# Optimization experiments

Hardware: AMD Instinct MI355X
Metric: run time of the kernel (lower is better)

Reference implementation:

```python
import jax, jax.numpy as jnp
import numpy as np

B, S, D = 8, 2048, 1024

def setup_inputs() -> dict:
    key = jax.random.key(0)
    ks = jax.random.split(key, 7)
    x = jax.random.normal(ks[0], (B, S, D), dtype=jnp.float32)
    s = 1.0 / np.sqrt(D)
    Wq = jax.random.normal(ks[1], (D, D), dtype=jnp.float32) * s
    bq = jax.random.normal(ks[2], (D,), dtype=jnp.float32) * 0.01
    Wk = jax.random.normal(ks[3], (D, D), dtype=jnp.float32) * s
    bk = jax.random.normal(ks[4], (D,), dtype=jnp.float32) * 0.01
    Wv = jax.random.normal(ks[5], (D, D), dtype=jnp.float32) * s
    bv = jax.random.normal(ks[6], (D,), dtype=jnp.float32) * 0.01
    return {"x": x, "Wq": Wq, "bq": bq, "Wk": Wk, "bk": bk, "Wv": Wv, "bv": bv}

def reference(x, Wq, bq, Wk, bk, Wv, bv):
    # QKV projections: [B,S,D]
    Q = jnp.einsum('bsd,de->bse', x, Wq) + bq
    K = jnp.einsum('bsd,de->bse', x, Wk) + bk
    V = jnp.einsum('bsd,de->bse', x, Wv) + bv
    scale = 1.0 / jnp.sqrt(jnp.asarray(Q.shape[-1], Q.dtype))
    attn = jnp.einsum('bqd,bkd->bqk', Q, K) * scale  # [B,S,S]
    attn = jax.nn.softmax(attn, axis=-1)
    return jnp.einsum('bqk,bkd->bqd', attn, V)
```

## Files before the change

### kernel.cpp

```cpp
#include <hip/hip_runtime.h>
#include <cstdint>


#define Bb 8
#define Ss 2048
#define Dd 1024

typedef unsigned short ushort_t;
typedef __attribute__((ext_vector_type(8))) short short8;
typedef __attribute__((ext_vector_type(4))) float floatx4;

__device__ inline ushort_t f2bf(float f) {
    unsigned int u = __float_as_uint(f);
    unsigned int r = (u + 0x7fffu + ((u >> 16) & 1u)) >> 16;
    return (ushort_t)r;
}
__device__ inline float bf2f(ushort_t u) {
    return __uint_as_float(((unsigned int)u) << 16);
}

__device__ inline floatx4 mfma16(short8 a, short8 b, floatx4 c) {
    return __builtin_amdgcn_mfma_f32_16x16x32_bf16(a, b, c, 0, 0, 0);
}

__device__ inline void gload16(const void* g, void* l) {
    __builtin_amdgcn_global_load_lds(
        (const __attribute__((address_space(1))) void*)g,
        (__attribute__((address_space(3))) void*)l, 16, 0, 0);
}

__device__ __attribute__((always_inline)) void gemm_core256(
    const ushort_t* __restrict__ A, const ushort_t* __restrict__ B,
    int K, int lda, int ldb, int m0, int n0, int tid,
    ushort_t* lds, floatx4 acc[8][4])
{
    const int lane = tid & 63;
    const int wave = tid >> 6;
    const int l3   = lane >> 3;
    const int kc   = ((lane & 7) ^ l3) * 8;

    const ushort_t* aS[2][2];
    const ushort_t* bS[2][2];
#pragma unroll
    for (int i = 0; i < 2; i++) {
#pragma unroll
        for (int g = 0; g < 2; g++) {
            const int r = i * 128 + g * 64 + wave * 8 + l3;
            aS[g][i] = A + (size_t)(m0 + r) * lda + kc;
        }
#pragma unroll
        for (int nh = 0; nh < 2; nh++) {
            const int c = wave + i * 8;
            const int r = (c >> 2) * 64 + nh * 32 + (c & 3) * 8 + l3;
            bS[nh][i] = B + (size_t)(n0 + r) * ldb + kc;
        }
    }

    const int jA   = (wave >> 2) * 64 + (lane & 15);
    const int jB   = (wave & 3) * 32 + (lane & 15);
    const int swz0 = (((lane >> 4) + 0) ^ (lane & 7)) * 8;
    const int swz1 = (((lane >> 4) + 4) ^ (lane & 7)) * 8;

#define STG(DST, REGI, SRC, KOFS)                                             \
    do {                                                                      \
        gload16(SRC[0] + (KOFS), (DST) + (REGI) * 8192 + wave * 512);         \
        gload16(SRC[1] + (KOFS), (DST) + (REGI) * 8192 + (wave + 8) * 512);   \
    } while (0)

#define PHASE(MH, NH, STGSTMT, VMSTMT)                                        \
    do {                                                                      \
        const ushort_t* ba  = cb + (MH) * 8192;                               \
        const ushort_t* bb2 = cb + (2 + (NH)) * 8192;                         \
        short8 af[4][2], bf[2][2];                                            \
        _Pragma("unroll")                                                     \
        for (int mi = 0; mi < 4; mi++) {                                      \
            af[mi][0] = *(const short8*)&ba[(jA + mi * 16) * 64 + swz0];      \
            af[mi][1] = *(const short8*)&ba[(jA + mi * 16) * 64 + swz1];      \
        }                                                                     \
        _Pragma("unroll")                                                     \
        for (int ni = 0; ni < 2; ni++) {                                      \
            bf[ni][0] = *(const short8*)&bb2[(jB + ni * 16) * 64 + swz0];     \
            bf[ni][1] = *(const short8*)&bb2[(jB + ni * 16) * 64 + swz1];     \
        }                                                                     \
        STGSTMT;                                                              \
        __builtin_amdgcn_sched_barrier(0);                                    \
        __builtin_amdgcn_s_barrier();                                         \
        asm volatile("s_waitcnt lgkmcnt(0)" ::: "memory");                    \
        __builtin_amdgcn_sched_barrier(0);                                    \
        __builtin_amdgcn_s_setprio(1);                                        \
        _Pragma("unroll")                                                     \
        for (int ks = 0; ks < 2; ks++)                                        \
            _Pragma("unroll")                                                 \
            for (int mi = 0; mi < 4; mi++)                                    \
                _Pragma("unroll")                                             \
                for (int ni = 0; ni < 2; ni++)                                \
                    acc[(MH) * 4 + mi][(NH) * 2 + ni] = mfma16(               \
                        af[mi][ks], bf[ni][ks],                               \
                        acc[(MH) * 4 + mi][(NH) * 2 + ni]);                   \
        __builtin_amdgcn_s_setprio(0);                                        \
        __builtin_amdgcn_sched_barrier(0);                                    \
        VMSTMT;                                                               \
        __builtin_amdgcn_s_barrier();                                         \
        __builtin_amdgcn_sched_barrier(0);                                    \
    } while (0)

    STG(lds, 0, aS[0], 0);
    STG(lds, 1, aS[1], 0);
    STG(lds, 2, bS[0], 0);
    STG(lds, 3, bS[1], 0);
    STG(lds + 32768, 2, bS[0], 64);
    STG(lds + 32768, 0, aS[0], 64);
    asm volatile("s_waitcnt vmcnt(4)" ::: "memory");
    __builtin_amdgcn_s_barrier();
    __builtin_amdgcn_sched_barrier(0);

    const int NT = K >> 6;
    for (int t = 0; t < NT; t++) {
        const ushort_t* cb = lds + (t & 1) * 32768;
        ushort_t* nb = lds + ((t + 1) & 1) * 32768;
        ushort_t* sb = lds + (t & 1) * 32768;
        const int k1 = (t + 1 < NT ? t + 1 : 0) << 6;
        const int k2 = (t + 2 < NT ? t + 2 : 0) << 6;
        PHASE(0, 0, STG(nb, 1, aS[1], k1), (void)0);
        PHASE(1, 0, STG(nb, 3, bS[1], k1), (void)0);
        PHASE(0, 1, STG(sb, 2, bS[0], k2), (void)0);
        PHASE(1, 1, STG(sb, 0, aS[0], k2),
              asm volatile("s_waitcnt vmcnt(4)" ::: "memory"));
    }
    asm volatile("s_waitcnt vmcnt(0)" ::: "memory");
#undef PHASE
#undef STG
}

template <int EPI>
__global__ __launch_bounds__(512, 2) void gemm256(
    const ushort_t* __restrict__ A, const ushort_t* __restrict__ B,
    void* __restrict__ Cv, float* __restrict__ aux,
    int K, int lda, int ldb, int ldc,
    size_t strideA, size_t strideB, size_t strideC)
{
    const int z = blockIdx.z;
    A += (size_t)z * strideA;
    B += (size_t)z * strideB;
    const int m0 = blockIdx.y * 256;
    const int n0 = blockIdx.x * 256;

    __shared__ __align__(16) ushort_t lds[2 * 4 * 8192];

    floatx4 acc[8][4] = {};
    gemm_core256(A, B, K, lda, ldb, m0, n0, (int)threadIdx.x, lds, acc);

    const int lane = threadIdx.x & 63;
    const int wave = threadIdx.x >> 6;
    const int row0 = m0 + (wave >> 2) * 128 + (lane >> 4) * 4;
    const int col0 = n0 + (wave & 3) * 64 + (lane & 15);

    if (EPI == 0) {
        ushort_t* Cb = (ushort_t*)Cv;
        float bval[4];
#pragma unroll
        for (int nf = 0; nf < 4; nf++) bval[nf] = aux[col0 + nf * 16];
#pragma unroll
        for (int mf = 0; mf < 8; mf++)
#pragma unroll
            for (int i = 0; i < 4; i++) {
                const size_t ro = (size_t)(row0 + mf * 16 + i) * ldc;
#pragma unroll
                for (int nf = 0; nf < 4; nf++)
                    Cb[ro + col0 + nf * 16] = f2bf(acc[mf][nf][i] + bval[nf]);
            }
    } else if (EPI == 1) {
        ushort_t* Cb = (ushort_t*)Cv + (size_t)z * strideC;
        float* ls = aux + z * Ss;
        float rs[8][4];
#pragma unroll
        for (int mf = 0; mf < 8; mf++)
#pragma unroll
            for (int i = 0; i < 4; i++) rs[mf][i] = 0.f;
#pragma unroll
        for (int mf = 0; mf < 8; mf++)
#pragma unroll
            for (int i = 0; i < 4; i++) {
                const size_t ro = (size_t)(row0 + mf * 16 + i) * ldc;
#pragma unroll
                for (int nf = 0; nf < 4; nf++) {
                    const ushort_t o = f2bf(__expf(acc[mf][nf][i] * 0.03125f));
                    Cb[ro + col0 + nf * 16] = o;
                    rs[mf][i] += bf2f(o);
                }
            }
#pragma unroll
        for (int mf = 0; mf < 8; mf++)
#pragma unroll
            for (int i = 0; i < 4; i++) {
                float s = rs[mf][i];
                s += __shfl_xor(s, 1);
                s += __shfl_xor(s, 2);
                s += __shfl_xor(s, 4);
                s += __shfl_xor(s, 8);
                rs[mf][i] = s;
            }
        if ((lane & 15) == 0) {
#pragma unroll
            for (int mf = 0; mf < 8; mf++)
#pragma unroll
                for (int i = 0; i < 4; i++)
                    atomicAdd(&ls[row0 + mf * 16 + i], rs[mf][i]);
        }
    } else {
        float* Cf = (float*)Cv + (size_t)z * strideC;
#pragma unroll
        for (int mf = 0; mf < 8; mf++)
#pragma unroll
            for (int i = 0; i < 4; i++) {
                const int gr = row0 + mf * 16 + i;
                const float iv = 1.0f / aux[z * Ss + gr];
#pragma unroll
                for (int nf = 0; nf < 4; nf++)
                    Cf[(size_t)gr * ldc + col0 + nf * 16] = acc[mf][nf][i] * iv;
            }
    }
}

__global__ __launch_bounds__(256) void vtrans(
    const ushort_t* __restrict__ QKVb, ushort_t* __restrict__ Vt)
{
    __shared__ __align__(16) ushort_t tile[64][72];
    const int t = blockIdx.x;
    const int z = t >> 9, rem = t & 511;
    const int d0 = (rem & 15) * 64, s0 = (rem >> 4) * 64;
    const int tid = threadIdx.x;
    const int rr = tid >> 3;
    const int c8 = (tid & 7) * 8;
#pragma unroll
    for (int i = 0; i < 2; i++) {
        const int s = s0 + rr + i * 32;
        uint4 v = *(const uint4*)&QKVb[((size_t)(z * Ss + s)) * 3072 + 2048 + d0 + c8];
        *(uint4*)&tile[rr + i * 32][c8] = v;
    }
    __syncthreads();
#pragma unroll
    for (int i = 0; i < 2; i++) {
        const int d = rr + i * 32;
        ushort_t u[8];
#pragma unroll
        for (int j = 0; j < 8; j++) u[j] = tile[c8 + j][d];
        *(uint4*)&Vt[(size_t)z * Dd * Ss + (size_t)(d0 + d) * Ss + s0 + c8] =
            *(const uint4*)u;
    }
}

__global__ __launch_bounds__(256) void prep(
    const float* __restrict__ x,
    const float* __restrict__ W0, const float* __restrict__ W1,
    const float* __restrict__ W2,
    const float* __restrict__ bq, const float* __restrict__ bk,
    const float* __restrict__ bv,
    ushort_t* __restrict__ xb, ushort_t* __restrict__ Wall,
    float* __restrict__ ball)
{
    const int bid = blockIdx.x;
    const int tid = threadIdx.x;

    if (bid < 8192) {
        const size_t i = (size_t)bid * 256 + tid;
        const float4* p = (const float4*)x + i * 2;
        float4 a = p[0], b = p[1];
        ushort_t u[8];
        u[0]=f2bf(a.x); u[1]=f2bf(a.y); u[2]=f2bf(a.z); u[3]=f2bf(a.w);
        u[4]=f2bf(b.x); u[5]=f2bf(b.y); u[6]=f2bf(b.z); u[7]=f2bf(b.w);
        *(uint4*)(xb + i * 8) = *(const uint4*)u;
    } else if (bid < 8960) {
        const int t = bid - 8192;
        const int z = t >> 8;
        const float* W = (z == 0) ? W0 : (z == 1) ? W1 : W2;
        ushort_t* Wt = Wall + (size_t)z * Dd * Dd;
        __shared__ float tt[64][65];
        const int n0 = ((t >> 4) & 15) * 64, k0 = (t & 15) * 64;
        const int r  = tid >> 4;
        const int c4 = (tid & 15) * 4;
#pragma unroll
        for (int i = 0; i < 4; i++) {
            float4 v = *(const float4*)&W[(size_t)(k0 + r + i * 16) * Dd + n0 + c4];
            tt[r + i * 16][c4 + 0] = v.x;
            tt[r + i * 16][c4 + 1] = v.y;
            tt[r + i * 16][c4 + 2] = v.z;
            tt[r + i * 16][c4 + 3] = v.w;
        }
        __syncthreads();
#pragma unroll
        for (int i = 0; i < 4; i++) {
            const int rn = r + i * 16;
            ushort_t u[4];
#pragma unroll
            for (int j = 0; j < 4; j++) u[j] = f2bf(tt[c4 + j][rn]);
            *(uint2*)&Wt[(size_t)(n0 + rn) * Dd + k0 + c4] = *(const uint2*)u;
        }
    } else {
#pragma unroll
        for (int j = 0; j < 12; j++) {
            const int idx = j * 256 + tid;
            float v = (idx < 1024) ? bq[idx]
                    : (idx < 2048) ? bk[idx - 1024] : bv[idx - 2048];
            ball[idx] = v;
        }
    }
}

extern "C" void kernel_launch(void* const* d_in, const int* in_sizes, int n_in,
                              void* d_out, int out_size, void* d_ws, size_t ws_size,
                              hipStream_t stream)
{
    const float* x  = (const float*)d_in[0];
    const float* Wq = (const float*)d_in[1];
    const float* bq = (const float*)d_in[2];
    const float* Wk = (const float*)d_in[3];
    const float* bk = (const float*)d_in[4];
    const float* Wv = (const float*)d_in[5];
    const float* bv = (const float*)d_in[6];
    float* out = (float*)d_out;

    char* ws = (char*)d_ws;
    const size_t MB = 1u << 20;
    ushort_t* xb   = (ushort_t*)(ws);
    ushort_t* Vt   = (ushort_t*)(ws);
    ushort_t* QKVb = (ushort_t*)(ws + 32 * MB);
    ushort_t* Pb   = (ushort_t*)(ws + 128 * MB);
    float*    lsum = (float*)(ws + 192 * MB);
    ushort_t* Wall = (ushort_t*)d_out;
    float*    ball = (float*)((char*)d_out + 6 * MB);

    prep<<<8961, 256, 0, stream>>>(x, Wq, Wk, Wv, bq, bk, bv, xb, Wall, ball);

    dim3 g1(3072 / 256, 16384 / 256, 1);
    gemm256<0><<<g1, 512, 0, stream>>>(xb, Wall, QKVb, ball,
                                       Dd, Dd, Dd, 3072, 0, 0, 0);

    hipMemsetAsync(lsum, 0, (size_t)Bb * Ss * sizeof(float), stream);
    vtrans<<<4096, 256, 0, stream>>>(QKVb, Vt);
    dim3 g2(Ss / 256, Ss / 256, Bb);
    gemm256<1><<<g2, 512, 0, stream>>>(QKVb, QKVb + 1024, Pb, lsum,
                                       Dd, 3072, 3072, Ss,
                                       (size_t)Ss * 3072, (size_t)Ss * 3072,
                                       (size_t)Ss * Ss);

    dim3 g3(Dd / 256, Ss / 256, Bb);
    gemm256<3><<<g3, 512, 0, stream>>>(Pb, Vt, out, lsum,
                                       Ss, Ss, Ss, Dd,
                                       (size_t)Ss * Ss, (size_t)Dd * Ss,
                                       (size_t)Ss * Dd);
}
```

Before: 405.2 us.

## Reuse LDS fragments across GEMM phases via serpentine quadrant order

Hoists the A/B fragment registers out of each phase and reorders the four quadrant phases (00,10,11,01) so each phase reloads only one operand half from LDS instead of both. This cuts LDS read traffic per K-tile. The prefetch schedule is reshuffled so each freed LDS slot is refilled right after its last reader. It risks a race if any slot is overwritten while a later phase still reads it.

```diff
diff --git a/kernel.cpp b/kernel.cpp
--- a/kernel.cpp
+++ b/kernel.cpp
@@ -60,6 +60,8 @@
     const int jB   = (wave & 3) * 32 + (lane & 15);
     const int swz0 = (((lane >> 4) + 0) ^ (lane & 7)) * 8;
     const int swz1 = (((lane >> 4) + 4) ^ (lane & 7)) * 8;
+
+    short8 aF[4][2], bF[2][2];
 
 #define STG(DST, REGI, SRC, KOFS)                                             \
     do {                                                                      \
@@ -67,39 +69,46 @@
         gload16(SRC[1] + (KOFS), (DST) + (REGI) * 8192 + (wave + 8) * 512);   \
     } while (0)
 
-#define PHASE(MH, NH, STGSTMT, VMSTMT)                                        \
+#define RD_A(QM)                                                              \
+    _Pragma("unroll")                                                         \
+    for (int mi = 0; mi < 4; mi++) {                                          \
+        const ushort_t* pA_ = cb + (QM) * 8192 + (jA + mi * 16) * 64;         \
+        aF[mi][0] = *(const short8*)&pA_[swz0];                               \
+        aF[mi][1] = *(const short8*)&pA_[swz1];                               \
+    }
+
+#define RD_B(QN)                                                              \
+    _Pragma("unroll")                                                         \
+    for (int ni = 0; ni < 2; ni++) {                                          \
+        const ushort_t* pB_ = cb + (2 + (QN)) * 8192 + (jB + ni * 16) * 64;   \
+        bF[ni][0] = *(const short8*)&pB_[swz0];                               \
+        bF[ni][1] = *(const short8*)&pB_[swz1];                               \
+    }
+
+#define MM(QM, QN)                                                            \
+    _Pragma("unroll")                                                         \
+    for (int ks = 0; ks < 2; ks++)                                            \
+        _Pragma("unroll")                                                     \
+        for (int mi = 0; mi < 4; mi++)                                        \
+            _Pragma("unroll")                                                 \
+            for (int ni = 0; ni < 2; ni++)                                    \
+                acc[(QM) * 4 + mi][(QN) * 2 + ni] =                           \
+                    mfma16(aF[mi][ks], bF[ni][ks],                            \
+                           acc[(QM) * 4 + mi][(QN) * 2 + ni]);
+
+#define PHASE(RDS, MMS, STGS, VMS)                                            \
     do {                                                                      \
-        const ushort_t* ba  = cb + (MH) * 8192;                               \
-        const ushort_t* bb2 = cb + (2 + (NH)) * 8192;                         \
-        short8 af[4][2], bf[2][2];                                            \
-        _Pragma("unroll")                                                     \
-        for (int mi = 0; mi < 4; mi++) {                                      \
-            af[mi][0] = *(const short8*)&ba[(jA + mi * 16) * 64 + swz0];      \
-            af[mi][1] = *(const short8*)&ba[(jA + mi * 16) * 64 + swz1];      \
-        }                                                                     \
-        _Pragma("unroll")                                                     \
-        for (int ni = 0; ni < 2; ni++) {                                      \
-            bf[ni][0] = *(const short8*)&bb2[(jB + ni * 16) * 64 + swz0];     \
-            bf[ni][1] = *(const short8*)&bb2[(jB + ni * 16) * 64 + swz1];     \
-        }                                                                     \
-        STGSTMT;                                                              \
+        RDS                                                                   \
+        STGS;                                                                 \
         __builtin_amdgcn_sched_barrier(0);                                    \
         __builtin_amdgcn_s_barrier();                                         \
         asm volatile("s_waitcnt lgkmcnt(0)" ::: "memory");                    \
         __builtin_amdgcn_sched_barrier(0);                                    \
         __builtin_amdgcn_s_setprio(1);                                        \
-        _Pragma("unroll")                                                     \
-        for (int ks = 0; ks < 2; ks++)                                        \
-            _Pragma("unroll")                                                 \
-            for (int mi = 0; mi < 4; mi++)                                    \
-                _Pragma("unroll")                                             \
-                for (int ni = 0; ni < 2; ni++)                                \
-                    acc[(MH) * 4 + mi][(NH) * 2 + ni] = mfma16(               \
-                        af[mi][ks], bf[ni][ks],                               \
-                        acc[(MH) * 4 + mi][(NH) * 2 + ni]);                   \
+        MMS                                                                   \
         __builtin_amdgcn_s_setprio(0);                                        \
         __builtin_amdgcn_sched_barrier(0);                                    \
-        VMSTMT;                                                               \
+        VMS;                                                                  \
         __builtin_amdgcn_s_barrier();                                         \
         __builtin_amdgcn_sched_barrier(0);                                    \
     } while (0)
@@ -109,7 +118,7 @@
     STG(lds, 2, bS[0], 0);
     STG(lds, 3, bS[1], 0);
     STG(lds + 32768, 2, bS[0], 64);
-    STG(lds + 32768, 0, aS[0], 64);
+    STG(lds + 32768, 1, aS[1], 64);
     asm volatile("s_waitcnt vmcnt(4)" ::: "memory");
     __builtin_amdgcn_s_barrier();
     __builtin_amdgcn_sched_barrier(0);
@@ -121,14 +130,17 @@
         ushort_t* sb = lds + (t & 1) * 32768;
         const int k1 = (t + 1 < NT ? t + 1 : 0) << 6;
         const int k2 = (t + 2 < NT ? t + 2 : 0) << 6;
-        PHASE(0, 0, STG(nb, 1, aS[1], k1), (void)0);
-        PHASE(1, 0, STG(nb, 3, bS[1], k1), (void)0);
-        PHASE(0, 1, STG(sb, 2, bS[0], k2), (void)0);
-        PHASE(1, 1, STG(sb, 0, aS[0], k2),
+        PHASE(RD_A(0) RD_B(0), MM(0, 0), STG(nb, 3, bS[1], k1), (void)0);
+        PHASE(RD_A(1),         MM(1, 0), STG(nb, 0, aS[0], k1), (void)0);
+        PHASE(RD_B(1),         MM(1, 1), STG(sb, 2, bS[0], k2), (void)0);
+        PHASE(RD_A(0),         MM(0, 1), STG(sb, 1, aS[1], k2),
               asm volatile("s_waitcnt vmcnt(4)" ::: "memory"));
     }
     asm volatile("s_waitcnt vmcnt(0)" ::: "memory");
 #undef PHASE
+#undef MM
+#undef RD_B
+#undef RD_A
 #undef STG
 }
 
```

After: 398.2 us. Within noise of the previous version (-1.7%).
